# Optimization experiments

Hardware: AMD Instinct MI355X
Metric: run time of the kernel (lower is better)

Reference implementation:

```python
import jax, jax.numpy as jnp
import numpy as np

EPS = 1e-8

def _fft_unit_proj(x):
    # Project each vector to unit magnitude in the Fourier domain (norm_kv=True).
    f = jnp.fft.fft(x, axis=-1)
    return jnp.real(jnp.fft.ifft(f / (jnp.abs(f) + EPS), axis=-1))

def _hrr_key_value_query(k, v, q, causal=True):
    # k, v, q: [B, S, D]
    k = _fft_unit_proj(k)
    v = _fft_unit_proj(v)
    # bind: circular convolution of key and value
    kv = jnp.real(jnp.fft.ifft(jnp.fft.fft(k, axis=-1) * jnp.fft.fft(v, axis=-1), axis=-1))
    # causal associative memory: running sum of bound pairs along sequence
    if causal:
        mem = jnp.cumsum(kv, axis=1)
    else:
        mem = jnp.broadcast_to(jnp.sum(kv, axis=1, keepdims=True), kv.shape)
    # unbind: circular correlation of memory with query
    out = jnp.real(jnp.fft.ifft(jnp.conj(jnp.fft.fft(q, axis=-1)) * jnp.fft.fft(mem, axis=-1), axis=-1))
    return out


def setup_inputs() -> dict:
    key = jax.random.key(0)
    ks = jax.random.split(key, 8)
    B, S, D = 2, 4096, 2048
    sc = 1.0 / np.sqrt(D).astype(np.float32)
    return {
        "hidden_states": jax.random.normal(ks[0], (B, S, D), jnp.float32),
        "base_output": jax.random.normal(ks[1], (B, S, D), jnp.float32),
        "Wq": jax.random.normal(ks[2], (D, D), jnp.float32) * sc,
        "bq": jnp.zeros((D,), jnp.float32),
        "Wk": jax.random.normal(ks[3], (D, D), jnp.float32) * sc,
        "bk": jnp.zeros((D,), jnp.float32),
        "Wv": jax.random.normal(ks[4], (D, D), jnp.float32) * sc,
        "bv": jnp.zeros((D,), jnp.float32),
        "gate": jax.random.normal(ks[5], (1,), jnp.float32) * 0.1,
    }


def reference(hidden_states, base_output, Wq, bq, Wk, bk, Wv, bv, gate):
    # Adapter q/k/v projections (nn.Linear uses y = x @ W.T + b)
    q = jnp.einsum('bsd,ed->bse', hidden_states, Wq) + bq
    k = jnp.einsum('bsd,ed->bse', hidden_states, Wk) + bk
    v = jnp.einsum('bsd,ed->bse', hidden_states, Wv) + bv
    adapter = _hrr_key_value_query(k, v, q, causal=True)
    return base_output + gate * adapter
```

## Files before the change

kernel.cpp:

```cpp
#include <hip/hip_runtime.h>
#include <math.h>

constexpr int D_DIM  = 2048;
constexpr int HALF_D = 1024;
constexpr int B_DIM  = 2;
constexpr int S_DIM  = 4096;
constexpr int NROW   = B_DIM * S_DIM;
constexpr int NCHUNK = 64;
constexpr int CHLEN  = S_DIM / NCHUNK;
constexpr float EPS_ = 1e-8f;

typedef __attribute__((ext_vector_type(8))) short  short8;
typedef __attribute__((ext_vector_type(8))) unsigned short ushort8;
typedef __attribute__((ext_vector_type(4))) float  f32x4;

__device__ __forceinline__ float2 mkf2(float x, float y){ float2 r; r.x=x; r.y=y; return r; }
__device__ __forceinline__ float2 cmulf(float2 a, float2 b){
  return mkf2(fmaf(a.x, b.x, -a.y*b.y), fmaf(a.x, b.y, a.y*b.x));
}
__device__ __forceinline__ unsigned short f2bf(float x){
  unsigned u = __float_as_uint(x);
  u += 0x7fff + ((u >> 16) & 1);
  return (unsigned short)(u >> 16);
}
__device__ __forceinline__ float bf2f(unsigned short h){
  return __uint_as_float(((unsigned)h) << 16);
}

__global__ __launch_bounds__(256)
void cvt_inputs(const float* __restrict__ hs, const float* __restrict__ Wq,
                const float* __restrict__ Wk, const float* __restrict__ Wv,
                unsigned short* __restrict__ hsb, unsigned short* __restrict__ wb)
{
  constexpr int n8 = (NROW * D_DIM) / 8;
  constexpr int w8 = (D_DIM * D_DIM) / 8;
  int i = blockIdx.x * 256 + threadIdx.x;
  const float* src;
  unsigned short* dst;
  int local;
  if (i < n8) { src = hs; local = i; dst = hsb + (size_t)i * 8; }
  else {
    int j = i - n8;
    int seg = j >> 19;
    local = j & (w8 - 1);
    src = (seg == 0) ? Wq : (seg == 1) ? Wk : Wv;
    dst = wb + (size_t)j * 8;
  }
  const float4* p = (const float4*)src + (size_t)local * 2;
  float4 a = p[0], b = p[1];
  ushort8 o;
  o[0]=f2bf(a.x); o[1]=f2bf(a.y); o[2]=f2bf(a.z); o[3]=f2bf(a.w);
  o[4]=f2bf(b.x); o[5]=f2bf(b.y); o[6]=f2bf(b.z); o[7]=f2bf(b.w);
  *(ushort8*)dst = o;
}

__global__ __launch_bounds__(512, 2)
void gemm_fused(const unsigned short* __restrict__ A,
                const unsigned short* __restrict__ Wc,
                const float* __restrict__ bq, const float* __restrict__ bk,
                const float* __restrict__ bv,
                unsigned short* __restrict__ qb, unsigned short* __restrict__ kvb)
{
  constexpr int K = 2048, NITER = 16;
  __shared__ unsigned short lds[65536];
  const int tid  = threadIdx.x;
  const int wid  = tid >> 6, lane = tid & 63;
  const int wr   = wid >> 2, wc = wid & 3;

  int bid = blockIdx.x;
  int sw  = (bid & 7) * 96 + (bid >> 3);
  const int bm = (sw / 24) * 256, bn = (sw % 24) * 256;

  const int srow = tid >> 3;
  const int skc  = ((tid & 7) ^ (srow & 7)) * 8;
  const unsigned short* Ag = A  + (size_t)(bm + srow) * K + skc;
  const unsigned short* Bg = Wc + (size_t)(bn + srow) * K + skc;
  unsigned short* Al = lds;
  unsigned short* Bl = lds + 32768;
  const int stoff = wid * 512;

  auto stA = [&](int kt, int d, int h, int r) {
    __builtin_amdgcn_global_load_lds(
      (const __attribute__((address_space(1))) void*)(Ag + (size_t)(h * 128 + r * 64) * K + kt * 64),
      (__attribute__((address_space(3))) void*)(Al + d * 16384 + h * 8192 + r * 4096 + stoff),
      16, 0, 0);
  };
  auto stB = [&](int kt, int d, int h, int r) {
    __builtin_amdgcn_global_load_lds(
      (const __attribute__((address_space(1))) void*)(Bg + (size_t)(h * 128 + r * 64) * K + kt * 64),
      (__attribute__((address_space(3))) void*)(Bl + d * 16384 + h * 8192 + r * 4096 + stoff),
      16, 0, 0);
  };

  const int frow = lane & 15;
  const int kq   = lane >> 4;
  int ksw[2];
  ksw[0] = ((0 * 4 + kq) ^ (frow & 7)) * 8;
  ksw[1] = ((1 * 4 + kq) ^ (frow & 7)) * 8;
  const int arow0 = (wr * 128 + frow) * 64;
  const int brow0 = (wc * 64 + frow) * 64;

  f32x4 acc[8][4];
#pragma unroll
  for (int i = 0; i < 8; ++i)
#pragma unroll
    for (int j = 0; j < 4; ++j) acc[i][j] = (f32x4){0.f, 0.f, 0.f, 0.f};

  stA(0, 0, 0, 0); stA(0, 0, 0, 1); stA(0, 0, 1, 0); stA(0, 0, 1, 1);
  stB(0, 0, 0, 0); stB(0, 0, 0, 1); stB(0, 0, 1, 0); stB(0, 0, 1, 1);
  stB(1, 1, 0, 0); stB(1, 1, 0, 1); stB(1, 1, 1, 0); stB(1, 1, 1, 1);
  asm volatile("s_waitcnt vmcnt(4)" ::: "memory");
  __builtin_amdgcn_s_barrier();
  __builtin_amdgcn_sched_barrier(0);

#pragma unroll 1
  for (int it = 0; it < NITER; ++it) {
    const bool nl = (it < NITER - 1);
    const int t1 = 2 * it + 1;
    short8 bfr[8];
#pragma unroll
    for (int ph = 0; ph < 8; ++ph) {
      const int g  = ph & 3;
      const int db = ph >> 2;
      const unsigned short* Ab = Al + db * 16384;
      const unsigned short* Bb = Bl + db * 16384;

      if      (ph == 0) { stA(t1, 1, 0, 0); stA(t1, 1, 0, 1); }
      else if (ph == 1) { stA(t1, 1, 1, 0); stA(t1, 1, 1, 1); }
      else if (ph == 2) { if (nl) { stB(t1 + 1, 0, 0, 0); stB(t1 + 1, 0, 0, 1); } }
      else if (ph == 3) { if (nl) { stB(t1 + 1, 0, 1, 0); stB(t1 + 1, 0, 1, 1); } }
      else if (ph == 4) { if (nl) { stA(t1 + 1, 0, 0, 0); stA(t1 + 1, 0, 0, 1); } }
      else if (ph == 5) { if (nl) { stA(t1 + 1, 0, 1, 0); stA(t1 + 1, 0, 1, 1); } }
      else if (ph == 6) { if (nl) { stB(t1 + 2, 1, 0, 0); stB(t1 + 2, 1, 0, 1); } }
      else              { if (nl) { stB(t1 + 2, 1, 1, 0); stB(t1 + 2, 1, 1, 1); } }

      short8 af[2][2];
#pragma unroll
      for (int q = 0; q < 2; ++q)
#pragma unroll
        for (int ks = 0; ks < 2; ++ks)
          af[q][ks] = *(const short8*)(Ab + arow0 + (2 * g + q) * 1024 + ksw[ks]);
      if (g == 0) {
#pragma unroll
        for (int nf = 0; nf < 4; ++nf)
#pragma unroll
          for (int ks = 0; ks < 2; ++ks)
            bfr[nf * 2 + ks] = *(const short8*)(Bb + brow0 + nf * 1024 + ksw[ks]);
      }

      __builtin_amdgcn_s_barrier();
      asm volatile("s_waitcnt lgkmcnt(0)" ::: "memory");
      __builtin_amdgcn_sched_barrier(0);
      __builtin_amdgcn_s_setprio(1);
#pragma unroll
      for (int ks = 0; ks < 2; ++ks)
#pragma unroll
        for (int q = 0; q < 2; ++q)
#pragma unroll
          for (int nf = 0; nf < 4; ++nf)
            acc[2 * g + q][nf] = __builtin_amdgcn_mfma_f32_16x16x32_bf16(
                af[q][ks], bfr[nf * 2 + ks], acc[2 * g + q][nf], 0, 0, 0);
      __builtin_amdgcn_s_setprio(0);

      if (ph == 3) {
        if (nl) asm volatile("s_waitcnt vmcnt(4)" ::: "memory");
        else    asm volatile("s_waitcnt vmcnt(0)" ::: "memory");
      } else if (ph == 7) {
        if (nl) asm volatile("s_waitcnt vmcnt(4)" ::: "memory");
      }
      __builtin_amdgcn_s_barrier();
    }
  }

  const int seg = bn >> 11;
  const float* bp = (seg == 0) ? bq : (seg == 1) ? bk : bv;
  float bias_j[4];
#pragma unroll
  for (int j = 0; j < 4; ++j)
    bias_j[j] = bp[(bn + wc * 64 + j * 16 + frow) & 2047];
  const int er = (lane >> 4) * 4;
  unsigned short* dst = (seg == 0) ? qb : kvb;
  const size_t rstride = (seg == 0) ? 2048 : 4096;
  const int coff = (seg == 2) ? 2048 : 0;
#pragma unroll
  for (int I = 0; I < 8; ++I) {
    int row = bm + wr * 128 + I * 16 + er;
#pragma unroll
    for (int j = 0; j < 4; ++j) {
      int col = (bn + wc * 64 + j * 16 + frow) & 2047;
#pragma unroll
      for (int r = 0; r < 4; ++r) {
        float val = acc[I][j][r] + bias_j[j];
        dst[(size_t)(row + r) * rstride + coff + col] = f2bf(val);
      }
    }
  }
}

__device__ __forceinline__ int XS(int i){ return i ^ (((i >> 5) ^ (i >> 10)) & 31); }
__device__ __forceinline__ int TS(int i){ return i ^ ((i >> 5) & 31); }

__device__ __forceinline__ float2 mulmi(float2 w){ return mkf2(w.y, -w.x); }
__device__ __forceinline__ float2 mulw8(float2 w){
  const float c = 0.70710678118654752f;
  return mkf2(c * (w.x + w.y), c * (w.y - w.x));
}
__device__ __forceinline__ void bfly(float2& a, float2& b, float2 w){
  float2 v = cmulf(w, b);
  b = mkf2(a.x - v.x, a.y - v.y);
  a = mkf2(a.x + v.x, a.y + v.y);
}
__device__ __forceinline__ void bflyc(float2& a, float2& b, float2 w){
  float2 d = mkf2(a.x - b.x, a.y - b.y);
  a = mkf2(a.x + b.x, a.y + b.y);
  b = mkf2(fmaf(d.x, w.x, d.y * w.y), fmaf(d.y, w.x, -d.x * w.y));
}

__device__ __forceinline__ void fwd8(float2 e[8], float2 wA, float2 wB0, float2 wC0){
  bfly(e[0], e[1], wA); bfly(e[2], e[3], wA); bfly(e[4], e[5], wA); bfly(e[6], e[7], wA);
  float2 wB1 = mulmi(wB0);
  bfly(e[0], e[2], wB0); bfly(e[1], e[3], wB1); bfly(e[4], e[6], wB0); bfly(e[5], e[7], wB1);
  float2 wC1 = mulw8(wC0), wC2 = mulmi(wC0), wC3 = mulmi(wC1);
  bfly(e[0], e[4], wC0); bfly(e[1], e[5], wC1); bfly(e[2], e[6], wC2); bfly(e[3], e[7], wC3);
}
__device__ __forceinline__ void inv8(float2 e[8], float2 wA, float2 wB0, float2 wC0){
  float2 wC1 = mulw8(wC0), wC2 = mulmi(wC0), wC3 = mulmi(wC1);
  bflyc(e[0], e[4], wC0); bflyc(e[1], e[5], wC1); bflyc(e[2], e[6], wC2); bflyc(e[3], e[7], wC3);
  float2 wB1 = mulmi(wB0);
  bflyc(e[0], e[2], wB0); bflyc(e[1], e[3], wB1); bflyc(e[4], e[6], wB0); bflyc(e[5], e[7], wB1);
  bflyc(e[0], e[1], wA); bflyc(e[2], e[3], wA); bflyc(e[4], e[5], wA); bflyc(e[6], e[7], wA);
}

__device__ __forceinline__ float2 twld(const float* twr, const float* twi, int i){
  int s = TS(i);
  return mkf2(twr[s], twi[s]);
}

__device__ void fft_fwd(float2* X, const float* twr, const float* twi, int t)
{
  const float2 one = mkf2(1.f, 0.f);
  {
    int b = 8 * t;
    float2 e[8];
#pragma unroll
    for (int r = 0; r < 8; ++r) e[r] = X[XS(b + r)];
    fwd8(e, one, one, one);
#pragma unroll
    for (int r = 0; r < 8; ++r) X[XS(b + r)] = e[r];
  }
  __syncthreads();
  {
    int u = t >> 5, b = 64 * (t & 31) + u;
    float2 e[8];
#pragma unroll
    for (int r = 0; r < 8; ++r) e[r] = X[XS(b + 8 * r)];
    fwd8(e, twld(twr,twi,128*u), twld(twr,twi,64*u), twld(twr,twi,32*u));
#pragma unroll
    for (int r = 0; r < 8; ++r) X[XS(b + 8 * r)] = e[r];
  }
  __syncthreads();
  {
    int u = t & 63, b = 512 * (t >> 6) + u;
    float2 e[8];
#pragma unroll
    for (int r = 0; r < 8; ++r) e[r] = X[XS(b + 64 * r)];
    fwd8(e, twld(twr,twi,16*u), twld(twr,twi,8*u), twld(twr,twi,4*u));
#pragma unroll
    for (int r = 0; r < 8; ++r) X[XS(b + 64 * r)] = e[r];
  }
  __syncthreads();
#pragma unroll
  for (int h = 0; h < 2; ++h) {
    int u = t + 256 * h;
    float2 f[4];
#pragma unroll
    for (int r = 0; r < 4; ++r) f[r] = X[XS(u + 512 * r)];
    float2 wA = twld(twr,twi,2*u), wB0 = twld(twr,twi,u), wB1 = mulmi(wB0);
    bfly(f[0], f[1], wA);  bfly(f[2], f[3], wA);
    bfly(f[0], f[2], wB0); bfly(f[1], f[3], wB1);
#pragma unroll
    for (int r = 0; r < 4; ++r) X[XS(u + 512 * r)] = f[r];
  }
  __syncthreads();
}

__device__ void fft_inv(float2* X, const float* twr, const float* twi, int t)
{
  const float2 one = mkf2(1.f, 0.f);
#pragma unroll
  for (int h = 0; h < 2; ++h) {
    int u = t + 256 * h;
    float2 f[4];
#pragma unroll
    for (int r = 0; r < 4; ++r) f[r] = X[XS(u + 512 * r)];
    float2 wA = twld(twr,twi,2*u), wB0 = twld(twr,twi,u), wB1 = mulmi(wB0);
    bflyc(f[0], f[2], wB0); bflyc(f[1], f[3], wB1);
    bflyc(f[0], f[1], wA);  bflyc(f[2], f[3], wA);
#pragma unroll
    for (int r = 0; r < 4; ++r) X[XS(u + 512 * r)] = f[r];
  }
  __syncthreads();
  {
    int u = t & 63, b = 512 * (t >> 6) + u;
    float2 e[8];
#pragma unroll
    for (int r = 0; r < 8; ++r) e[r] = X[XS(b + 64 * r)];
    inv8(e, twld(twr,twi,16*u), twld(twr,twi,8*u), twld(twr,twi,4*u));
#pragma unroll
    for (int r = 0; r < 8; ++r) X[XS(b + 64 * r)] = e[r];
  }
  __syncthreads();
  {
    int u = t >> 5, b = 64 * (t & 31) + u;
    float2 e[8];
#pragma unroll
    for (int r = 0; r < 8; ++r) e[r] = X[XS(b + 8 * r)];
    inv8(e, twld(twr,twi,128*u), twld(twr,twi,64*u), twld(twr,twi,32*u));
#pragma unroll
    for (int r = 0; r < 8; ++r) X[XS(b + 8 * r)] = e[r];
  }
  __syncthreads();
  {
    int b = 8 * t;
    float2 e[8];
#pragma unroll
    for (int r = 0; r < 8; ++r) e[r] = X[XS(b + r)];
    inv8(e, one, one, one);
#pragma unroll
    for (int r = 0; r < 8; ++r) X[XS(b + r)] = e[r];
  }
  __syncthreads();
}

__global__ __launch_bounds__(256)
void twiddle_init(float2* __restrict__ twg)
{
  int i = blockIdx.x * 256 + threadIdx.x;
  if (i < HALF_D) {
    float sv, cv;
    sincosf(-6.283185307179586f * (float)i / (float)D_DIM, &sv, &cv);
    twg[i] = mkf2(cv, sv);
  }
}

__global__ __launch_bounds__(256)
void fftkv_kernel(unsigned short* __restrict__ kvb, const float2* __restrict__ twg)
{
  __shared__ float2 X[D_DIM];
  __shared__ float twr[HALF_D], twi[HALF_D];
  const int t = threadIdx.x;
  const size_t row = blockIdx.x;
  const unsigned short* kvrow = kvb + row * 4096;

  for (int i = t; i < HALF_D; i += 256) {
    float2 w = twg[i]; int s = TS(i); twr[s] = w.x; twi[s] = w.y;
  }
  {
    int i0 = t * 8;
    ushort8 k8 = *(const ushort8*)(kvrow + i0);
    ushort8 v8 = *(const ushort8*)(kvrow + 2048 + i0);
#pragma unroll
    for (int r = 0; r < 8; ++r) {
      int i = i0 + r;
      int p = __brev((unsigned)i) >> 21;
      X[XS(p)] = mkf2(bf2f(k8[r]), bf2f(v8[r]));
    }
  }
  __syncthreads();
  fft_fwd(X, twr, twi, t);

  unsigned int* outp = (unsigned int*)(kvb + row * 4096);
  for (int d = t; d < HALF_D; d += 256) {
    float2 p;
    if (d == 0) {
      float2 z0 = X[XS(0)], zn = X[XS(HALF_D)];
      float k0 = z0.x, v0 = z0.y, kn = zn.x, vn = zn.y;
      float p0 = (k0 / (fabsf(k0) + EPS_)) * (v0 / (fabsf(v0) + EPS_));
      float pn = (kn / (fabsf(kn) + EPS_)) * (vn / (fabsf(vn) + EPS_));
      p = mkf2(p0, pn);
    } else {
      float2 A = X[XS(d)];
      float2 Bc = X[XS(D_DIM - d)];
      float2 Bj = mkf2(Bc.x, -Bc.y);
      float2 Fk = mkf2(0.5f * (A.x + Bj.x), 0.5f * (A.y + Bj.y));
      float2 tt = mkf2(0.5f * (A.x - Bj.x), 0.5f * (A.y - Bj.y));
      float2 Fv = mkf2(tt.y, -tt.x);
      float sa = 1.f / (sqrtf(Fk.x*Fk.x + Fk.y*Fk.y) + EPS_);
      float sb = 1.f / (sqrtf(Fv.x*Fv.x + Fv.y*Fv.y) + EPS_);
      p = cmulf(Fk, Fv);
      float sc = sa * sb;
      p.x *= sc; p.y *= sc;
    }
    outp[d] = (unsigned)f2bf(p.x) | ((unsigned)f2bf(p.y) << 16);
  }
}

__global__ __launch_bounds__(256)
void scan_partial(const unsigned short* __restrict__ kvb, float2* __restrict__ part)
{
  int gid = blockIdx.x * 256 + threadIdx.x;
  int q4 = gid & 255;
  int chunk = (gid >> 8) & (NCHUNK - 1);
  int b = gid >> 14;
  const unsigned short* p = kvb + (size_t)(b * S_DIM + chunk * CHLEN) * 4096 + q4 * 8;
  float ar[4] = {0,0,0,0}, ai[4] = {0,0,0,0};
  for (int s = 0; s < CHLEN; ++s) {
    ushort8 v = *(const ushort8*)(p + (size_t)s * 4096);
#pragma unroll
    for (int e = 0; e < 4; ++e) { ar[e] += bf2f(v[2*e]); ai[e] += bf2f(v[2*e+1]); }
  }
  float2* pp = part + (size_t)(b * NCHUNK + chunk) * HALF_D + q4 * 4;
#pragma unroll
  for (int e = 0; e < 4; ++e) pp[e] = mkf2(ar[e], ai[e]);
}

__global__ __launch_bounds__(256)
void scan_offsets(float2* __restrict__ part)
{
  int gid = blockIdx.x * 256 + threadIdx.x;
  int d = gid & (HALF_D - 1);
  int b = gid >> 10;
  float2* p = part + (size_t)b * (NCHUNK * HALF_D) + d;
  float2 acc = mkf2(0.f, 0.f);
  for (int c = 0; c < NCHUNK; ++c) {
    float2 v = p[(size_t)c * HALF_D];
    p[(size_t)c * HALF_D] = acc;
    acc.x += v.x; acc.y += v.y;
  }
}

__global__ __launch_bounds__(256)
void scan_apply(unsigned short* __restrict__ kvb, const float2* __restrict__ part)
{
  int gid = blockIdx.x * 256 + threadIdx.x;
  int q4 = gid & 255;
  int chunk = (gid >> 8) & (NCHUNK - 1);
  int b = gid >> 14;
  unsigned short* p = kvb + (size_t)(b * S_DIM + chunk * CHLEN) * 4096 + q4 * 8;
  const float2* pp = part + (size_t)(b * NCHUNK + chunk) * HALF_D + q4 * 4;
  float ar[4], ai[4];
#pragma unroll
  for (int e = 0; e < 4; ++e) { float2 v = pp[e]; ar[e] = v.x; ai[e] = v.y; }
  for (int s = 0; s < CHLEN; ++s) {
    ushort8 v = *(const ushort8*)(p + (size_t)s * 4096);
    ushort8 o;
#pragma unroll
    for (int e = 0; e < 4; ++e) {
      ar[e] += bf2f(v[2*e]); ai[e] += bf2f(v[2*e+1]);
      o[2*e] = f2bf(ar[e]); o[2*e+1] = f2bf(ai[e]);
    }
    *(ushort8*)(p + (size_t)s * 4096) = o;
  }
}

__global__ __launch_bounds__(256)
void final_kernel(const unsigned short* __restrict__ qb,
                  const unsigned short* __restrict__ kvb,
                  const float* __restrict__ base, const float* __restrict__ gate,
                  const float2* __restrict__ twg, float* __restrict__ out)
{
  __shared__ float2 X[D_DIM];
  __shared__ float twr[HALF_D], twi[HALF_D];
  const int t = threadIdx.x;
  const size_t row0 = (size_t)blockIdx.x * 2;
  const unsigned short* qrow = qb + row0 * 2048;
  const unsigned short* m0 = kvb + row0 * 4096;
  const unsigned short* m1 = m0 + 4096;

  for (int i = t; i < HALF_D; i += 256) {
    float2 w = twg[i]; int s = TS(i); twr[s] = w.x; twi[s] = w.y;
  }
  {
    int i0 = t * 8;
    ushort8 q0 = *(const ushort8*)(qrow + i0);
    ushort8 q1 = *(const ushort8*)(qrow + 2048 + i0);
#pragma unroll
    for (int r = 0; r < 8; ++r) {
      int i = i0 + r;
      int p = __brev((unsigned)i) >> 21;
      X[XS(p)] = mkf2(bf2f(q0[r]), bf2f(q1[r]));
    }
  }
  __syncthreads();
  fft_fwd(X, twr, twi, t);

  for (int d = t; d < HALF_D; d += 256) {
    if (d == 0) {
      float2 z0 = X[XS(0)], zn = X[XS(HALF_D)];
      float M00 = bf2f(m0[0]), M0N = bf2f(m0[1]);
      float M10 = bf2f(m1[0]), M1N = bf2f(m1[1]);
      X[XS(0)]      = mkf2(z0.x * M00, z0.y * M10);
      X[XS(HALF_D)] = mkf2(zn.x * M0N, zn.y * M1N);
    } else {
      float2 Zd = X[XS(d)];
      float2 Zn = X[XS(D_DIM - d)];
      float2 Fq0 = mkf2(0.5f * (Zd.x + Zn.x), 0.5f * (Zd.y - Zn.y));
      float2 td  = mkf2(0.5f * (Zd.x - Zn.x), 0.5f * (Zd.y + Zn.y));
      float2 Fq1 = mkf2(td.y, -td.x);
      float2 M0d = mkf2(bf2f(m0[2*d]), bf2f(m0[2*d+1]));
      float2 M1d = mkf2(bf2f(m1[2*d]), bf2f(m1[2*d+1]));
      float2 G0 = mkf2(Fq0.x*M0d.x + Fq0.y*M0d.y, Fq0.x*M0d.y - Fq0.y*M0d.x);
      float2 G1 = mkf2(Fq1.x*M1d.x + Fq1.y*M1d.y, Fq1.x*M1d.y - Fq1.y*M1d.x);
      X[XS(d)]         = mkf2(G0.x - G1.y, G0.y + G1.x);
      X[XS(D_DIM - d)] = mkf2(G0.x + G1.y, G1.x - G0.y);
    }
  }
  __syncthreads();
  fft_inv(X, twr, twi, t);

  const float gv = gate[0] * (1.f / (float)D_DIM);
  const float* brow = base + row0 * 2048;
  float* orow = out + row0 * 2048;
  for (int i = t; i < D_DIM; i += 256) {
    int p = __brev((unsigned)i) >> 21;
    float2 y = X[XS(p)];
    orow[i]        = brow[i]        + gv * y.x;
    orow[2048 + i] = brow[2048 + i] + gv * y.y;
  }
}

extern "C" void kernel_launch(void* const* d_in, const int* in_sizes, int n_in,
                              void* d_out, int out_size, void* d_ws, size_t ws_size,
                              hipStream_t stream)
{
  const float* hs   = (const float*)d_in[0];
  const float* base = (const float*)d_in[1];
  const float* Wq   = (const float*)d_in[2];
  const float* bq   = (const float*)d_in[3];
  const float* Wk   = (const float*)d_in[4];
  const float* bk   = (const float*)d_in[5];
  const float* Wv   = (const float*)d_in[6];
  const float* bv   = (const float*)d_in[7];
  const float* gate = (const float*)d_in[8];
  float* out  = (float*)d_out;

  char* ws = (char*)d_ws;
  unsigned short* hsb = (unsigned short*)ws;
  unsigned short* wqb = (unsigned short*)(ws + 33554432);
  unsigned short* kvb = (unsigned short*)(ws + 58720256);
  unsigned short* qb  = (unsigned short*)(ws + 58720256 + 67108864);
  float2* part = (float2*)(ws + 58720256 + 67108864 + 33554432);
  float2* twg  = (float2*)ws;

  {
    constexpr int n8 = (NROW * D_DIM) / 8;
    constexpr int w8 = (D_DIM * D_DIM) / 8;
    cvt_inputs<<<(n8 + 3 * w8) / 256, 256, 0, stream>>>(hs, Wq, Wk, Wv, hsb, wqb);
  }

  gemm_fused<<<768, 512, 0, stream>>>(hsb, wqb, bq, bk, bv, qb, kvb);

  twiddle_init<<<4, 256, 0, stream>>>(twg);

  fftkv_kernel<<<NROW, 256, 0, stream>>>(kvb, twg);

  scan_partial<<<128, 256, 0, stream>>>(kvb, part);
  scan_offsets<<<(B_DIM * HALF_D) / 256, 256, 0, stream>>>(part);
  scan_apply<<<128, 256, 0, stream>>>(kvb, part);

  final_kernel<<<NROW / 2, 256, 0, stream>>>(qb, kvb, base, gate, twg, out);
}
```

Baseline: 351.3 us.

## Restructure QKV GEMM mainloop to triple-buffered BK=32 pipeline

Replaces the double-buffered BK=64 mainloop (8 phases per iteration, a barrier after each phase) with a three-stage ring buffer of BK=32 tiles. The loop prefetches two tiles ahead, interleaves the global-to-LDS loads with LDS fragment reads and MFMA groups, and uses one barrier per k-step. LDS use drops from 128KB to 96KB and the swizzle pattern changes to fit the narrower rows. The change is meant to cut barrier and wait stalls, at the cost of twice as many k iterations and a more delicate vmcnt and synchronization scheme.

```diff
diff --git a/kernel.cpp b/kernel.cpp
--- a/kernel.cpp
+++ b/kernel.cpp
@@ -61,8 +61,8 @@
                 const float* __restrict__ bv,
                 unsigned short* __restrict__ qb, unsigned short* __restrict__ kvb)
 {
-  constexpr int K = 2048, NITER = 16;
-  __shared__ unsigned short lds[65536];
+  constexpr int K = 2048, NT = 64;
+  __shared__ unsigned short lds[49152];
   const int tid  = threadIdx.x;
   const int wid  = tid >> 6, lane = tid & 63;
   const int wr   = wid >> 2, wc = wid & 3;
@@ -71,34 +71,32 @@
   int sw  = (bid & 7) * 96 + (bid >> 3);
   const int bm = (sw / 24) * 256, bn = (sw % 24) * 256;
 
-  const int srow = tid >> 3;
-  const int skc  = ((tid & 7) ^ (srow & 7)) * 8;
+  const int srow = tid >> 2;
+  const int skc  = ((tid & 3) ^ ((tid >> 3) & 3)) * 8;
   const unsigned short* Ag = A  + (size_t)(bm + srow) * K + skc;
   const unsigned short* Bg = Wc + (size_t)(bn + srow) * K + skc;
   unsigned short* Al = lds;
-  unsigned short* Bl = lds + 32768;
+  unsigned short* Bl = lds + 24576;
   const int stoff = wid * 512;
 
-  auto stA = [&](int kt, int d, int h, int r) {
+  auto stA = [&](int kt, int b, int r) {
     __builtin_amdgcn_global_load_lds(
-      (const __attribute__((address_space(1))) void*)(Ag + (size_t)(h * 128 + r * 64) * K + kt * 64),
-      (__attribute__((address_space(3))) void*)(Al + d * 16384 + h * 8192 + r * 4096 + stoff),
+      (const __attribute__((address_space(1))) void*)(Ag + (size_t)r * 128 * K + kt * 32),
+      (__attribute__((address_space(3))) void*)(Al + b * 8192 + r * 4096 + stoff),
       16, 0, 0);
   };
-  auto stB = [&](int kt, int d, int h, int r) {
+  auto stB = [&](int kt, int b, int r) {
     __builtin_amdgcn_global_load_lds(
-      (const __attribute__((address_space(1))) void*)(Bg + (size_t)(h * 128 + r * 64) * K + kt * 64),
-      (__attribute__((address_space(3))) void*)(Bl + d * 16384 + h * 8192 + r * 4096 + stoff),
+      (const __attribute__((address_space(1))) void*)(Bg + (size_t)r * 128 * K + kt * 32),
+      (__attribute__((address_space(3))) void*)(Bl + b * 8192 + r * 4096 + stoff),
       16, 0, 0);
   };
 
   const int frow = lane & 15;
   const int kq   = lane >> 4;
-  int ksw[2];
-  ksw[0] = ((0 * 4 + kq) ^ (frow & 7)) * 8;
-  ksw[1] = ((1 * 4 + kq) ^ (frow & 7)) * 8;
-  const int arow0 = (wr * 128 + frow) * 64;
-  const int brow0 = (wc * 64 + frow) * 64;
+  const int ksw  = (kq ^ ((frow >> 1) & 3)) * 8;
+  const int arow0 = (wr * 128 + frow) * 32 + ksw;
+  const int brow0 = (wc * 64 + frow) * 32 + ksw;
 
   f32x4 acc[8][4];
 #pragma unroll
@@ -106,70 +104,75 @@
 #pragma unroll
     for (int j = 0; j < 4; ++j) acc[i][j] = (f32x4){0.f, 0.f, 0.f, 0.f};
 
-  stA(0, 0, 0, 0); stA(0, 0, 0, 1); stA(0, 0, 1, 0); stA(0, 0, 1, 1);
-  stB(0, 0, 0, 0); stB(0, 0, 0, 1); stB(0, 0, 1, 0); stB(0, 0, 1, 1);
-  stB(1, 1, 0, 0); stB(1, 1, 0, 1); stB(1, 1, 1, 0); stB(1, 1, 1, 1);
+  stA(0, 0, 0); stA(0, 0, 1); stB(0, 0, 0); stB(0, 0, 1);
+  stA(1, 1, 0); stA(1, 1, 1); stB(1, 1, 0); stB(1, 1, 1);
   asm volatile("s_waitcnt vmcnt(4)" ::: "memory");
   __builtin_amdgcn_s_barrier();
   __builtin_amdgcn_sched_barrier(0);
 
+  int c = 0;
 #pragma unroll 1
-  for (int it = 0; it < NITER; ++it) {
-    const bool nl = (it < NITER - 1);
-    const int t1 = 2 * it + 1;
-    short8 bfr[8];
-#pragma unroll
-    for (int ph = 0; ph < 8; ++ph) {
-      const int g  = ph & 3;
-      const int db = ph >> 2;
-      const unsigned short* Ab = Al + db * 16384;
-      const unsigned short* Bb = Bl + db * 16384;
-
-      if      (ph == 0) { stA(t1, 1, 0, 0); stA(t1, 1, 0, 1); }
-      else if (ph == 1) { stA(t1, 1, 1, 0); stA(t1, 1, 1, 1); }
-      else if (ph == 2) { if (nl) { stB(t1 + 1, 0, 0, 0); stB(t1 + 1, 0, 0, 1); } }
-      else if (ph == 3) { if (nl) { stB(t1 + 1, 0, 1, 0); stB(t1 + 1, 0, 1, 1); } }
-      else if (ph == 4) { if (nl) { stA(t1 + 1, 0, 0, 0); stA(t1 + 1, 0, 0, 1); } }
-      else if (ph == 5) { if (nl) { stA(t1 + 1, 0, 1, 0); stA(t1 + 1, 0, 1, 1); } }
-      else if (ph == 6) { if (nl) { stB(t1 + 2, 1, 0, 0); stB(t1 + 2, 1, 0, 1); } }
-      else              { if (nl) { stB(t1 + 2, 1, 1, 0); stB(t1 + 2, 1, 1, 1); } }
-
-      short8 af[2][2];
-#pragma unroll
-      for (int q = 0; q < 2; ++q)
-#pragma unroll
-        for (int ks = 0; ks < 2; ++ks)
-          af[q][ks] = *(const short8*)(Ab + arow0 + (2 * g + q) * 1024 + ksw[ks]);
-      if (g == 0) {
-#pragma unroll
-        for (int nf = 0; nf < 4; ++nf)
-#pragma unroll
-          for (int ks = 0; ks < 2; ++ks)
-            bfr[nf * 2 + ks] = *(const short8*)(Bb + brow0 + nf * 1024 + ksw[ks]);
-      }
-
+  for (int kt = 0; kt < NT; ++kt) {
+    const unsigned short* Ab = Al + c * 8192;
+    const unsigned short* Bb = Bl + c * 8192;
+    int nb = c + 2; if (nb >= 3) nb -= 3;
+    const bool st = (kt < NT - 2);
+    short8 bfr[4], afe[2], afo[2];
+
+    if (st) stA(kt + 2, nb, 0);
+#pragma unroll
+    for (int nf = 0; nf < 4; ++nf) bfr[nf] = *(const short8*)(Bb + brow0 + nf * 512);
+    afe[0] = *(const short8*)(Ab + arow0);
+    afe[1] = *(const short8*)(Ab + arow0 + 512);
+
+    if (st) stA(kt + 2, nb, 1);
+    afo[0] = *(const short8*)(Ab + arow0 + 2 * 512);
+    afo[1] = *(const short8*)(Ab + arow0 + 3 * 512);
+    __builtin_amdgcn_s_setprio(1);
+#pragma unroll
+    for (int q = 0; q < 2; ++q)
+#pragma unroll
+      for (int nf = 0; nf < 4; ++nf)
+        acc[q][nf] = __builtin_amdgcn_mfma_f32_16x16x32_bf16(afe[q], bfr[nf], acc[q][nf], 0, 0, 0);
+    __builtin_amdgcn_s_setprio(0);
+
+    if (st) stB(kt + 2, nb, 0);
+    afe[0] = *(const short8*)(Ab + arow0 + 4 * 512);
+    afe[1] = *(const short8*)(Ab + arow0 + 5 * 512);
+    __builtin_amdgcn_s_setprio(1);
+#pragma unroll
+    for (int q = 0; q < 2; ++q)
+#pragma unroll
+      for (int nf = 0; nf < 4; ++nf)
+        acc[2 + q][nf] = __builtin_amdgcn_mfma_f32_16x16x32_bf16(afo[q], bfr[nf], acc[2 + q][nf], 0, 0, 0);
+    __builtin_amdgcn_s_setprio(0);
+
+    if (st) stB(kt + 2, nb, 1);
+    afo[0] = *(const short8*)(Ab + arow0 + 6 * 512);
+    afo[1] = *(const short8*)(Ab + arow0 + 7 * 512);
+    __builtin_amdgcn_s_setprio(1);
+#pragma unroll
+    for (int q = 0; q < 2; ++q)
+#pragma unroll
+      for (int nf = 0; nf < 4; ++nf)
+        acc[4 + q][nf] = __builtin_amdgcn_mfma_f32_16x16x32_bf16(afe[q], bfr[nf], acc[4 + q][nf], 0, 0, 0);
+    __builtin_amdgcn_s_setprio(0);
+
+    __builtin_amdgcn_s_setprio(1);
+#pragma unroll
+    for (int q = 0; q < 2; ++q)
+#pragma unroll
+      for (int nf = 0; nf < 4; ++nf)
+        acc[6 + q][nf] = __builtin_amdgcn_mfma_f32_16x16x32_bf16(afo[q], bfr[nf], acc[6 + q][nf], 0, 0, 0);
+    __builtin_amdgcn_s_setprio(0);
+
+    if (kt < NT - 1) {
+      if (kt < NT - 2) asm volatile("s_waitcnt vmcnt(4)" ::: "memory");
+      else             asm volatile("s_waitcnt vmcnt(0)" ::: "memory");
       __builtin_amdgcn_s_barrier();
-      asm volatile("s_waitcnt lgkmcnt(0)" ::: "memory");
       __builtin_amdgcn_sched_barrier(0);
-      __builtin_amdgcn_s_setprio(1);
-#pragma unroll
-      for (int ks = 0; ks < 2; ++ks)
-#pragma unroll
-        for (int q = 0; q < 2; ++q)
-#pragma unroll
-          for (int nf = 0; nf < 4; ++nf)
-            acc[2 * g + q][nf] = __builtin_amdgcn_mfma_f32_16x16x32_bf16(
-                af[q][ks], bfr[nf * 2 + ks], acc[2 * g + q][nf], 0, 0, 0);
-      __builtin_amdgcn_s_setprio(0);
-
-      if (ph == 3) {
-        if (nl) asm volatile("s_waitcnt vmcnt(4)" ::: "memory");
-        else    asm volatile("s_waitcnt vmcnt(0)" ::: "memory");
-      } else if (ph == 7) {
-        if (nl) asm volatile("s_waitcnt vmcnt(4)" ::: "memory");
-      }
-      __builtin_amdgcn_s_barrier();
-    }
+    }
+    c = (c == 2) ? 0 : c + 1;
   }
 
   const int seg = bn >> 11;
```

New measurement: 362.2 us. +3.1%, slower.
